# Performance work log

Hardware: AMD Instinct MI355X
Metric: run time of the kernel (lower is better)

The kernel has to match this reference:

```python
import jax, jax.numpy as jnp
import numpy as np

B, T, F, H = 128, 1024, 64, 256


def _lstm_step(h, c, x_t, W_ih, W_hh, b):
    # PyTorch gate order: i, f, g, o ; b = b_ih + b_hh
    g = x_t @ W_ih.T + h @ W_hh.T + b
    i, f, gg, o = jnp.split(g, 4, axis=-1)
    c_new = jax.nn.sigmoid(f) * c + jax.nn.sigmoid(i) * jnp.tanh(gg)
    h_new = jax.nn.sigmoid(o) * jnp.tanh(c_new)
    return h_new, c_new


def setup_inputs() -> dict:
    key = jax.random.key(0)
    ks = jax.random.split(key, 20)
    s = 1.0 / np.sqrt(H)
    u = lambda k, shape: jax.random.uniform(k, shape, jnp.float32, -s, s)
    return {
        "x": jax.random.normal(ks[0], (B, T, F), jnp.float32),
        "eps": jax.random.normal(ks[1], (1, B, H), jnp.float32),
        "enc_W_ih": u(ks[2], (4 * H, F)),
        "enc_W_hh": u(ks[3], (4 * H, H)),
        "enc_b": u(ks[4], (4 * H,)),
        "W_mp": u(ks[5], (H, H)),
        "b_mp": u(ks[6], (H,)),
        "W_lp": u(ks[7], (H, H)),
        "b_lp": u(ks[8], (H,)),
        "dec_W_ih": u(ks[9], (4 * H, H)),
        "dec_W_hh": u(ks[10], (4 * H, H)),
        "dec_b": u(ks[11], (4 * H,)),
        "W_mx": u(ks[12], (F, H)),
        "b_mx": u(ks[13], (F,)),
        "W_lx": u(ks[14], (F, H)),
        "b_lx": u(ks[15], (F,)),
    }


def reference(x, eps, enc_W_ih, enc_W_hh, enc_b, W_mp, b_mp, W_lp, b_lp,
              dec_W_ih, dec_W_hh, dec_b, W_mx, b_mx, W_lx, b_lx):
    Bx = x.shape[0]
    # ---- encoder LSTM over time ----
    def enc_step(carry, x_t):
        h, c = carry
        h, c = _lstm_step(h, c, x_t, enc_W_ih, enc_W_hh, enc_b)
        return (h, c), None
    h0 = jnp.zeros((Bx, H), x.dtype)
    (h_T, _), _ = jax.lax.scan(enc_step, (h0, h0), x.transpose(1, 0, 2))
    h_T = h_T[None]  # [1, B, H] like torch nn.LSTM final h

    # ---- posterior heads + reparameterization ----
    mu_post = h_T @ W_mp.T + b_mp
    logsigma2_post = h_T @ W_lp.T + b_lp
    z0 = eps * jnp.exp(logsigma2_post / 2) + mu_post  # [1, B, H]

    def dec_step(carry, _):
        y, h, c = carry
        h, c = _lstm_step(h, c, y, dec_W_ih, dec_W_hh, dec_b)
        return (h, h, c), h
    y0 = jnp.zeros((Bx, H), x.dtype)
    c0 = jnp.zeros((Bx, H), x.dtype)
    _, ys = jax.lax.scan(dec_step, (y0, z0[0], c0), None, length=T)
    outputs = ys.transpose(1, 0, 2)  # [B, T, H]

    mu_xhat = outputs @ W_mx.T + b_mx            # [B, T, F]
    logsigma2_xhat = outputs @ W_lx.T + b_lx     # [B, T, F]
    return (mu_post, logsigma2_post, mu_xhat, logsigma2_xhat)
```

## Files before the change

kernel.cpp:

```cpp
#include <hip/hip_runtime.h>
#include <stdint.h>

#define Bc 128
#define Tc 1024
#define Fc 64
#define Hc 256

typedef float f32x4 __attribute__((ext_vector_type(4)));
typedef short s16x8 __attribute__((ext_vector_type(8)));

#define MFMA16(a, b, c) __builtin_amdgcn_mfma_f32_16x16x32_bf16((a), (b), (c), 0, 0, 0)

__device__ unsigned long long g_hbuf[2 * Bc * Hc];

__device__ __forceinline__ unsigned short f2bf(float f) {
  unsigned u = __float_as_uint(f);
  u += 0x7FFFu + ((u >> 16) & 1u);
  return (unsigned short)(u >> 16);
}
__device__ __forceinline__ float bf2f(unsigned short h) {
  return __uint_as_float(((unsigned)h) << 16);
}
__device__ __forceinline__ float sigm(float x) { return 1.0f / (1.0f + __expf(-x)); }
__device__ __forceinline__ float tanh2(float x) { return 1.0f - 2.0f / (__expf(2.0f * x) + 1.0f); }

__device__ __forceinline__ void wfrag2(const float* p, s16x8& hi, s16x8& lo) {
#pragma unroll
  for (int j = 0; j < 8; ++j) {
    unsigned short h = f2bf(p[j]);
    hi[j] = (short)h;
    lo[j] = (short)f2bf(p[j] - bf2f(h));
  }
}
__device__ __forceinline__ void wfrag2sum(const float* p, const float* q, s16x8& hi, s16x8& lo) {
#pragma unroll
  for (int j = 0; j < 8; ++j) {
    float v = p[j] + q[j];
    unsigned short h = f2bf(v);
    hi[j] = (short)h;
    lo[j] = (short)f2bf(v - bf2f(h));
  }
}
__device__ __forceinline__ f32x4 splat4(float v) {
  f32x4 r; r[0] = v; r[1] = v; r[2] = v; r[3] = v; return r;
}

extern "C" __global__ void __launch_bounds__(256, 1)
vrae_persistent(const float* __restrict__ x, const float* __restrict__ eps,
                const float* __restrict__ Wih_e, const float* __restrict__ Whh_e,
                const float* __restrict__ b_e,
                const float* __restrict__ Wmp, const float* __restrict__ bmp,
                const float* __restrict__ Wlp, const float* __restrict__ blp,
                const float* __restrict__ Wih_d, const float* __restrict__ Whh_d,
                const float* __restrict__ b_d,
                const float* __restrict__ Wmx, const float* __restrict__ bmx,
                const float* __restrict__ Wlx, const float* __restrict__ blx,
                float* __restrict__ out)
{
  __shared__ unsigned short h_hi[16][264];
  __shared__ unsigned short h_lo[16][264];
  __shared__ unsigned short x_hi[16][72];
  __shared__ unsigned short x_lo[16][72];
  __shared__ float glds[4][16][36];

  unsigned long long* hbuf = g_hbuf;

  const int tid  = threadIdx.x;
  const int wg   = blockIdx.x;
  const int sg   = wg & 7;
  const int gg   = wg >> 3;
  const int wv   = tid >> 6;
  const int l15  = tid & 15;
  const int quad = (tid >> 4) & 3;
  const int s0   = sg * 16;
  const int um   = tid >> 4;
  const int uj   = tid & 15;

  auto consume = [&](int tag) {
    const unsigned long long* src =
        hbuf + (size_t)(tag & 1) * (Bc * Hc) + (size_t)(s0 + um) * Hc;
    unsigned long long w[16];
#pragma unroll
    for (int u = 0; u < 16; ++u)
      w[u] = __hip_atomic_load(src + uj + 16 * u, __ATOMIC_RELAXED, __HIP_MEMORY_SCOPE_AGENT);
    for (;;) {
      bool ok = true;
#pragma unroll
      for (int u = 0; u < 16; ++u) ok = ok && ((w[u] >> 32) == (unsigned long long)(unsigned)tag);
      if (ok) break;
      __builtin_amdgcn_s_sleep(2);
#pragma unroll
      for (int u = 0; u < 16; ++u)
        if ((w[u] >> 32) != (unsigned long long)(unsigned)tag)
          w[u] = __hip_atomic_load(src + uj + 16 * u, __ATOMIC_RELAXED, __HIP_MEMORY_SCOPE_AGENT);
    }
#pragma unroll
    for (int u = 0; u < 16; ++u) {
      h_hi[um][uj + 16 * u] = (unsigned short)(w[u] >> 16);
      h_lo[um][uj + 16 * u] = (unsigned short)(w[u] & 0xFFFFu);
    }
  };

  auto publish_h = [&](int otag, float hv, int jloc) {
    unsigned long long* dst =
        hbuf + (size_t)(otag & 1) * (Bc * Hc) + (size_t)(s0 + um) * Hc + gg * 32 + jloc;
    unsigned short hi = f2bf(hv);
    unsigned short lo = f2bf(hv - bf2f(hi));
    unsigned long long word = ((unsigned long long)(unsigned)otag << 32) |
                              (((unsigned)hi << 16) | (unsigned)lo);
    __hip_atomic_store(dst, word, __ATOMIC_RELAXED, __HIP_MEMORY_SCOPE_AGENT);
  };

  float creg0 = 0.f, creg1 = 0.f;
  auto lstm_update = [&](int otag) {
#pragma unroll
    for (int u = 0; u < 2; ++u) {
      const int j = uj + 16 * u;
      float gi = glds[0][um][j], gf = glds[1][um][j];
      float gc = glds[2][um][j], go = glds[3][um][j];
      float iv = sigm(gi), fv = sigm(gf), cv = tanh2(gc), ov = sigm(go);
      float cr = u ? creg1 : creg0;
      cr = fv * cr + iv * cv;
      float hv = ov * tanh2(cr);
      if (u) creg1 = cr; else creg0 = cr;
      publish_h(otag, hv, j);
    }
  };

  s16x8 wmh[2][8], wml[2][8];
  s16x8 wxh[2][2], wxl[2][2];
  float biasg[2];
#pragma unroll
  for (int ch = 0; ch < 2; ++ch) {
    const int row = wv * 256 + gg * 32 + ch * 16 + l15;
    biasg[ch] = b_e[row];
#pragma unroll
    for (int c = 0; c < 8; ++c)
      wfrag2(Whh_e + (size_t)row * Hc + c * 32 + quad * 8, wmh[ch][c], wml[ch][c]);
#pragma unroll
    for (int c = 0; c < 2; ++c)
      wfrag2(Wih_e + (size_t)row * Fc + c * 32 + quad * 8, wxh[ch][c], wxl[ch][c]);
  }

#pragma unroll
  for (int u = 0; u < 16; ++u) { h_hi[um][uj + 16 * u] = 0; h_lo[um][uj + 16 * u] = 0; }
  __syncthreads();

  for (int it = 0; it < Tc; ++it) {
    {
      const float* xp = x + (size_t)(s0 + um) * (Tc * Fc) + (size_t)it * Fc + uj * 4;
      f32x4 xv = *(const f32x4*)xp;
#pragma unroll
      for (int j = 0; j < 4; ++j) {
        unsigned short h = f2bf(xv[j]);
        x_hi[um][uj * 4 + j] = h;
        x_lo[um][uj * 4 + j] = f2bf(xv[j] - bf2f(h));
      }
    }
    if (it > 0) consume(it);
    __syncthreads();

    f32x4 acc0 = splat4(biasg[0]);
    f32x4 acc1 = splat4(biasg[1]);
#pragma unroll
    for (int c = 0; c < 2; ++c) {
      s16x8 ah = *(const s16x8*)&x_hi[l15][c * 32 + quad * 8];
      s16x8 al = *(const s16x8*)&x_lo[l15][c * 32 + quad * 8];
      acc0 = MFMA16(ah, wxh[0][c], acc0);
      acc0 = MFMA16(ah, wxl[0][c], acc0);
      acc0 = MFMA16(al, wxh[0][c], acc0);
      acc1 = MFMA16(ah, wxh[1][c], acc1);
      acc1 = MFMA16(ah, wxl[1][c], acc1);
      acc1 = MFMA16(al, wxh[1][c], acc1);
    }
#pragma unroll
    for (int c = 0; c < 8; ++c) {
      s16x8 ah = *(const s16x8*)&h_hi[l15][c * 32 + quad * 8];
      s16x8 al = *(const s16x8*)&h_lo[l15][c * 32 + quad * 8];
      acc0 = MFMA16(ah, wmh[0][c], acc0);
      acc0 = MFMA16(ah, wml[0][c], acc0);
      acc0 = MFMA16(al, wmh[0][c], acc0);
      acc1 = MFMA16(ah, wmh[1][c], acc1);
      acc1 = MFMA16(ah, wml[1][c], acc1);
      acc1 = MFMA16(al, wmh[1][c], acc1);
    }
#pragma unroll
    for (int r = 0; r < 4; ++r) {
      glds[wv][quad * 4 + r][l15]      = acc0[r];
      glds[wv][quad * 4 + r][16 + l15] = acc1[r];
    }
    __syncthreads();
    lstm_update(it + 1);
  }

  consume(Tc);
  {
    const float* WM = (wv < 2) ? Wmp : Wlp;
    const float* bM = (wv < 2) ? bmp : blp;
    const int prow = gg * 32 + (wv & 1) * 16 + l15;
    s16x8 wph[8], wpl[8];
#pragma unroll
    for (int c = 0; c < 8; ++c)
      wfrag2(WM + (size_t)prow * Hc + c * 32 + quad * 8, wph[c], wpl[c]);
    const float pb = bM[prow];
    __syncthreads();
    f32x4 acc = splat4(pb);
#pragma unroll
    for (int c = 0; c < 8; ++c) {
      s16x8 ah = *(const s16x8*)&h_hi[l15][c * 32 + quad * 8];
      s16x8 al = *(const s16x8*)&h_lo[l15][c * 32 + quad * 8];
      acc = MFMA16(ah, wph[c], acc);
      acc = MFMA16(ah, wpl[c], acc);
      acc = MFMA16(al, wph[c], acc);
    }
#pragma unroll
    for (int r = 0; r < 4; ++r)
      glds[wv >> 1][quad * 4 + r][(wv & 1) * 16 + l15] = acc[r];
    __syncthreads();
#pragma unroll
    for (int u = 0; u < 2; ++u) {
      const int j  = uj + 16 * u;
      const int jg = gg * 32 + j;
      float mu = glds[0][um][j];
      float lp = glds[1][um][j];
      float ev = eps[(size_t)(s0 + um) * Hc + jg];
      float z  = ev * __expf(0.5f * lp) + mu;
      out[(size_t)(s0 + um) * Hc + jg] = mu;
      out[(size_t)Bc * Hc + (size_t)(s0 + um) * Hc + jg] = lp;
      publish_h(Tc + 1, z, j);
    }
    creg0 = 0.f; creg1 = 0.f;
  }

#pragma unroll
  for (int ch = 0; ch < 2; ++ch) {
    const int row = wv * 256 + gg * 32 + ch * 16 + l15;
    biasg[ch] = b_d[row];
#pragma unroll
    for (int c = 0; c < 8; ++c)
      wfrag2sum(Wih_d + (size_t)row * Hc + c * 32 + quad * 8,
                Whh_d + (size_t)row * Hc + c * 32 + quad * 8,
                wmh[ch][c], wml[ch][c]);
  }
  s16x8 wpjh[8], wpjl[8];
  float pjb;
  {
    const float* WP = (gg < 4) ? Wmx : Wlx;
    const float* bP = (gg < 4) ? bmx : blx;
    const int prow = (gg & 3) * 16 + l15;
    pjb = bP[prow];
#pragma unroll
    for (int c = 0; c < 8; ++c)
      wfrag2(WP + (size_t)prow * Hc + c * 32 + quad * 8, wpjh[c], wpjl[c]);
  }
  const size_t outMu = (size_t)2 * Bc * Hc;
  const size_t outLs = outMu + (size_t)Bc * Tc * Fc;

  for (int it = 0; it <= Tc; ++it) {
    consume(Tc + 1 + it);
    __syncthreads();

    if (it < Tc) {
      f32x4 acc0 = splat4(biasg[0]);
      f32x4 acc1 = splat4(biasg[1]);
      if (it == 0) {
#pragma unroll
        for (int ch = 0; ch < 2; ++ch) {
          const int row = wv * 256 + gg * 32 + ch * 16 + l15;
#pragma unroll
          for (int c = 0; c < 8; ++c) {
            s16x8 wzh, wzl;
            wfrag2(Whh_d + (size_t)row * Hc + c * 32 + quad * 8, wzh, wzl);
            s16x8 ah = *(const s16x8*)&h_hi[l15][c * 32 + quad * 8];
            s16x8 al = *(const s16x8*)&h_lo[l15][c * 32 + quad * 8];
            f32x4& acc = ch ? acc1 : acc0;
            acc = MFMA16(ah, wzh, acc);
            acc = MFMA16(ah, wzl, acc);
            acc = MFMA16(al, wzh, acc);
          }
        }
      } else {
#pragma unroll
        for (int c = 0; c < 8; ++c) {
          s16x8 ah = *(const s16x8*)&h_hi[l15][c * 32 + quad * 8];
          s16x8 al = *(const s16x8*)&h_lo[l15][c * 32 + quad * 8];
          acc0 = MFMA16(ah, wmh[0][c], acc0);
          acc0 = MFMA16(ah, wml[0][c], acc0);
          acc0 = MFMA16(al, wmh[0][c], acc0);
          acc1 = MFMA16(ah, wmh[1][c], acc1);
          acc1 = MFMA16(ah, wml[1][c], acc1);
          acc1 = MFMA16(al, wmh[1][c], acc1);
        }
      }
#pragma unroll
      for (int r = 0; r < 4; ++r) {
        glds[wv][quad * 4 + r][l15]      = acc0[r];
        glds[wv][quad * 4 + r][16 + l15] = acc1[r];
      }
      __syncthreads();
      lstm_update(Tc + 2 + it);
    }

    if (it > 0 && wv == 0) {
      f32x4 acc = splat4(pjb);
#pragma unroll
      for (int c = 0; c < 8; ++c) {
        s16x8 ah = *(const s16x8*)&h_hi[l15][c * 32 + quad * 8];
        s16x8 al = *(const s16x8*)&h_lo[l15][c * 32 + quad * 8];
        acc = MFMA16(ah, wpjh[c], acc);
        acc = MFMA16(ah, wpjl[c], acc);
        acc = MFMA16(al, wpjh[c], acc);
      }
      const size_t base = (gg < 4) ? outMu : outLs;
      const int tout = it - 1;
      const int fcol = (gg & 3) * 16 + l15;
#pragma unroll
      for (int r = 0; r < 4; ++r) {
        const int m = quad * 4 + r;
        out[base + ((size_t)(s0 + m) * Tc + tout) * Fc + fcol] = acc[r];
      }
    }
    __syncthreads();
  }

  {
    const int atag = 2 * Tc + 2;
#pragma unroll
    for (int u = 0; u < 2; ++u) {
      unsigned long long* dst = hbuf + (size_t)(s0 + um) * Hc + gg * 32 + uj + 16 * u;
      __hip_atomic_store(dst, ((unsigned long long)(unsigned)atag << 32),
                         __ATOMIC_RELAXED, __HIP_MEMORY_SCOPE_AGENT);
    }
    consume(atag);
#pragma unroll
    for (int u = 0; u < 2; ++u) {
      unsigned long long* dst =
          hbuf + (size_t)(Bc * Hc) + (size_t)(s0 + um) * Hc + gg * 32 + uj + 16 * u;
      __hip_atomic_store(dst, 0ull, __ATOMIC_RELAXED, __HIP_MEMORY_SCOPE_AGENT);
    }
  }
}

extern "C" void kernel_launch(void* const* d_in, const int* in_sizes, int n_in,
                              void* d_out, int out_size, void* d_ws, size_t ws_size,
                              hipStream_t stream)
{
  (void)in_sizes; (void)n_in; (void)out_size; (void)d_ws; (void)ws_size;

  const float* x     = (const float*)d_in[0];
  const float* eps   = (const float*)d_in[1];
  const float* Wih_e = (const float*)d_in[2];
  const float* Whh_e = (const float*)d_in[3];
  const float* b_e   = (const float*)d_in[4];
  const float* Wmp   = (const float*)d_in[5];
  const float* bmp   = (const float*)d_in[6];
  const float* Wlp   = (const float*)d_in[7];
  const float* blp   = (const float*)d_in[8];
  const float* Wih_d = (const float*)d_in[9];
  const float* Whh_d = (const float*)d_in[10];
  const float* b_d   = (const float*)d_in[11];
  const float* Wmx   = (const float*)d_in[12];
  const float* bmx   = (const float*)d_in[13];
  const float* Wlx   = (const float*)d_in[14];
  const float* blx   = (const float*)d_in[15];
  float* out = (float*)d_out;

  void* args[] = { &x, &eps, &Wih_e, &Whh_e, &b_e, &Wmp, &bmp, &Wlp, &blp,
                   &Wih_d, &Whh_d, &b_d, &Wmx, &bmx, &Wlx, &blx, &out };
  hipError_t err = hipLaunchCooperativeKernel((void*)vrae_persistent, dim3(64), dim3(256),
                                              args, 0, stream);
  if (err != hipSuccess) {
    vrae_persistent<<<dim3(64), dim3(256), 0, stream>>>(
        x, eps, Wih_e, Whh_e, b_e, Wmp, bmp, Wlp, blp,
        Wih_d, Whh_d, b_d, Wmx, bmx, Wlx, blx, out);
  }
}
```

Before: 5.505 ms.

## Interleave gate rows per wave to do LSTM update in registers via shuffles

Weight rows are remapped so each wave's MFMA output holds all four gates for its own 8 hidden columns. The LSTM cell update then runs in registers using lane shuffles instead of staging gates through LDS, which removes one __syncthreads and the LDS round trip per step. h and x LDS buffers are double-buffered by step parity, which lets the trailing barrier in the decoder loop go, and the spin-wait sleep is shortened. The cost is that only half the lanes do the nonlinearity, and parity buffering must stay correct (the projection now reads h_hi[0] after the encoder).

```diff
diff --git a/kernel.cpp b/kernel.cpp
--- a/kernel.cpp
+++ b/kernel.cpp
@@ -57,11 +57,11 @@
                 const float* __restrict__ Wlx, const float* __restrict__ blx,
                 float* __restrict__ out)
 {
-  __shared__ unsigned short h_hi[16][264];
-  __shared__ unsigned short h_lo[16][264];
-  __shared__ unsigned short x_hi[16][72];
-  __shared__ unsigned short x_lo[16][72];
-  __shared__ float glds[4][16][36];
+  __shared__ unsigned short h_hi[2][16][264];
+  __shared__ unsigned short h_lo[2][16][264];
+  __shared__ unsigned short x_hi[2][16][72];
+  __shared__ unsigned short x_lo[2][16][72];
+  __shared__ float glds[2][16][36];
 
   unsigned long long* hbuf = g_hbuf;
 
@@ -75,10 +75,14 @@
   const int s0   = sg * 16;
   const int um   = tid >> 4;
   const int uj   = tid & 15;
+  const int colbase = gg * 32 + wv * 8;
+  const int rowf0 = ((l15 < 8) ? 0 : 256) + colbase + (l15 & 7);
+  const int rowf1 = ((l15 < 8) ? 512 : 768) + colbase + (l15 & 7);
 
   auto consume = [&](int tag) {
+    const int p = tag & 1;
     const unsigned long long* src =
-        hbuf + (size_t)(tag & 1) * (Bc * Hc) + (size_t)(s0 + um) * Hc;
+        hbuf + (size_t)p * (Bc * Hc) + (size_t)(s0 + um) * Hc;
     unsigned long long w[16];
 #pragma unroll
     for (int u = 0; u < 16; ++u)
@@ -88,7 +92,7 @@
 #pragma unroll
       for (int u = 0; u < 16; ++u) ok = ok && ((w[u] >> 32) == (unsigned long long)(unsigned)tag);
       if (ok) break;
-      __builtin_amdgcn_s_sleep(2);
+      __builtin_amdgcn_s_sleep(1);
 #pragma unroll
       for (int u = 0; u < 16; ++u)
         if ((w[u] >> 32) != (unsigned long long)(unsigned)tag)
@@ -96,12 +100,11 @@
     }
 #pragma unroll
     for (int u = 0; u < 16; ++u) {
-      h_hi[um][uj + 16 * u] = (unsigned short)(w[u] >> 16);
-      h_lo[um][uj + 16 * u] = (unsigned short)(w[u] & 0xFFFFu);
+      h_hi[p][um][uj + 16 * u] = (unsigned short)(w[u] >> 16);
+      h_lo[p][um][uj + 16 * u] = (unsigned short)(w[u] & 0xFFFFu);
     }
   };
-
-  auto publish_h = [&](int otag, float hv, int jloc) {
+  auto publish_w = [&](int otag, float hv, int jloc) {
     unsigned long long* dst =
         hbuf + (size_t)(otag & 1) * (Bc * Hc) + (size_t)(s0 + um) * Hc + gg * 32 + jloc;
     unsigned short hi = f2bf(hv);
@@ -111,86 +114,89 @@
     __hip_atomic_store(dst, word, __ATOMIC_RELAXED, __HIP_MEMORY_SCOPE_AGENT);
   };
 
-  float creg0 = 0.f, creg1 = 0.f;
-  auto lstm_update = [&](int otag) {
-#pragma unroll
-    for (int u = 0; u < 2; ++u) {
-      const int j = uj + 16 * u;
-      float gi = glds[0][um][j], gf = glds[1][um][j];
-      float gc = glds[2][um][j], go = glds[3][um][j];
-      float iv = sigm(gi), fv = sigm(gf), cv = tanh2(gc), ov = sigm(go);
-      float cr = u ? creg1 : creg0;
-      cr = fv * cr + iv * cv;
-      float hv = ov * tanh2(cr);
-      if (u) creg1 = cr; else creg0 = cr;
-      publish_h(otag, hv, j);
+  float creg[4] = {0.f, 0.f, 0.f, 0.f};
+  auto update_publish = [&](f32x4 acc0, f32x4 acc1, int otag) {
+    f32x4 r0, r1;
+#pragma unroll
+    for (int r = 0; r < 4; ++r) {
+      r0[r] = __shfl_xor(acc0[r], 8, 64);
+      r1[r] = __shfl_xor(acc1[r], 8, 64);
+    }
+    if (l15 < 8) {
+#pragma unroll
+      for (int r = 0; r < 4; ++r) {
+        float iv = sigm(acc0[r]), fv = sigm(r0[r]);
+        float gv = tanh2(acc1[r]), ov = sigm(r1[r]);
+        float c = fv * creg[r] + iv * gv;
+        creg[r] = c;
+        float hv = ov * tanh2(c);
+        unsigned short hi = f2bf(hv);
+        unsigned short lo = f2bf(hv - bf2f(hi));
+        unsigned long long word = ((unsigned long long)(unsigned)otag << 32) |
+                                  (((unsigned)hi << 16) | (unsigned)lo);
+        __hip_atomic_store(hbuf + (size_t)(otag & 1) * (Bc * Hc) +
+                               (size_t)(s0 + quad * 4 + r) * Hc + colbase + l15,
+                           word, __ATOMIC_RELAXED, __HIP_MEMORY_SCOPE_AGENT);
+      }
     }
   };
 
-  s16x8 wmh[2][8], wml[2][8];
-  s16x8 wxh[2][2], wxl[2][2];
-  float biasg[2];
-#pragma unroll
-  for (int ch = 0; ch < 2; ++ch) {
-    const int row = wv * 256 + gg * 32 + ch * 16 + l15;
-    biasg[ch] = b_e[row];
-#pragma unroll
-    for (int c = 0; c < 8; ++c)
-      wfrag2(Whh_e + (size_t)row * Hc + c * 32 + quad * 8, wmh[ch][c], wml[ch][c]);
-#pragma unroll
-    for (int c = 0; c < 2; ++c)
-      wfrag2(Wih_e + (size_t)row * Fc + c * 32 + quad * 8, wxh[ch][c], wxl[ch][c]);
-  }
-
-#pragma unroll
-  for (int u = 0; u < 16; ++u) { h_hi[um][uj + 16 * u] = 0; h_lo[um][uj + 16 * u] = 0; }
-  __syncthreads();
+  s16x8 bh0[8], bl0[8], bh1[8], bl1[8];
+  s16x8 xbh0[2], xbl0[2], xbh1[2], xbl1[2];
+  float bias0 = b_e[rowf0], bias1 = b_e[rowf1];
+#pragma unroll
+  for (int c = 0; c < 8; ++c) {
+    wfrag2(Whh_e + (size_t)rowf0 * Hc + c * 32 + quad * 8, bh0[c], bl0[c]);
+    wfrag2(Whh_e + (size_t)rowf1 * Hc + c * 32 + quad * 8, bh1[c], bl1[c]);
+  }
+#pragma unroll
+  for (int c = 0; c < 2; ++c) {
+    wfrag2(Wih_e + (size_t)rowf0 * Fc + c * 32 + quad * 8, xbh0[c], xbl0[c]);
+    wfrag2(Wih_e + (size_t)rowf1 * Fc + c * 32 + quad * 8, xbh1[c], xbl1[c]);
+  }
 
   for (int it = 0; it < Tc; ++it) {
+    const int p = it & 1;
     {
       const float* xp = x + (size_t)(s0 + um) * (Tc * Fc) + (size_t)it * Fc + uj * 4;
       f32x4 xv = *(const f32x4*)xp;
 #pragma unroll
       for (int j = 0; j < 4; ++j) {
         unsigned short h = f2bf(xv[j]);
-        x_hi[um][uj * 4 + j] = h;
-        x_lo[um][uj * 4 + j] = f2bf(xv[j] - bf2f(h));
+        x_hi[p][um][uj * 4 + j] = h;
+        x_lo[p][um][uj * 4 + j] = f2bf(xv[j] - bf2f(h));
       }
     }
     if (it > 0) consume(it);
     __syncthreads();
 
-    f32x4 acc0 = splat4(biasg[0]);
-    f32x4 acc1 = splat4(biasg[1]);
+    f32x4 acc0 = splat4(bias0);
+    f32x4 acc1 = splat4(bias1);
 #pragma unroll
     for (int c = 0; c < 2; ++c) {
-      s16x8 ah = *(const s16x8*)&x_hi[l15][c * 32 + quad * 8];
-      s16x8 al = *(const s16x8*)&x_lo[l15][c * 32 + quad * 8];
-      acc0 = MFMA16(ah, wxh[0][c], acc0);
-      acc0 = MFMA16(ah, wxl[0][c], acc0);
-      acc0 = MFMA16(al, wxh[0][c], acc0);
-      acc1 = MFMA16(ah, wxh[1][c], acc1);
-      acc1 = MFMA16(ah, wxl[1][c], acc1);
-      acc1 = MFMA16(al, wxh[1][c], acc1);
-    }
-#pragma unroll
-    for (int c = 0; c < 8; ++c) {
-      s16x8 ah = *(const s16x8*)&h_hi[l15][c * 32 + quad * 8];
-      s16x8 al = *(const s16x8*)&h_lo[l15][c * 32 + quad * 8];
-      acc0 = MFMA16(ah, wmh[0][c], acc0);
-      acc0 = MFMA16(ah, wml[0][c], acc0);
-      acc0 = MFMA16(al, wmh[0][c], acc0);
-      acc1 = MFMA16(ah, wmh[1][c], acc1);
-      acc1 = MFMA16(ah, wml[1][c], acc1);
-      acc1 = MFMA16(al, wmh[1][c], acc1);
-    }
-#pragma unroll
-    for (int r = 0; r < 4; ++r) {
-      glds[wv][quad * 4 + r][l15]      = acc0[r];
-      glds[wv][quad * 4 + r][16 + l15] = acc1[r];
-    }
-    __syncthreads();
-    lstm_update(it + 1);
+      s16x8 ah = *(const s16x8*)&x_hi[p][l15][c * 32 + quad * 8];
+      s16x8 al = *(const s16x8*)&x_lo[p][l15][c * 32 + quad * 8];
+      acc0 = MFMA16(ah, xbh0[c], acc0);
+      acc0 = MFMA16(ah, xbl0[c], acc0);
+      acc0 = MFMA16(al, xbh0[c], acc0);
+      acc1 = MFMA16(ah, xbh1[c], acc1);
+      acc1 = MFMA16(ah, xbl1[c], acc1);
+      acc1 = MFMA16(al, xbh1[c], acc1);
+    }
+    if (it > 0) {
+#pragma unroll
+      for (int c = 0; c < 8; ++c) {
+        s16x8 ah = *(const s16x8*)&h_hi[p][l15][c * 32 + quad * 8];
+        s16x8 al = *(const s16x8*)&h_lo[p][l15][c * 32 + quad * 8];
+        acc0 = MFMA16(ah, bh0[c], acc0);
+        acc0 = MFMA16(ah, bl0[c], acc0);
+        acc0 = MFMA16(al, bh0[c], acc0);
+        acc1 = MFMA16(ah, bh1[c], acc1);
+        acc1 = MFMA16(ah, bl1[c], acc1);
+        acc1 = MFMA16(al, bh1[c], acc1);
+      }
+    }
+    update_publish(acc0, acc1, it + 1);
   }
 
   consume(Tc);
@@ -207,8 +213,8 @@
     f32x4 acc = splat4(pb);
 #pragma unroll
     for (int c = 0; c < 8; ++c) {
-      s16x8 ah = *(const s16x8*)&h_hi[l15][c * 32 + quad * 8];
-      s16x8 al = *(const s16x8*)&h_lo[l15][c * 32 + quad * 8];
+      s16x8 ah = *(const s16x8*)&h_hi[0][l15][c * 32 + quad * 8];
+      s16x8 al = *(const s16x8*)&h_lo[0][l15][c * 32 + quad * 8];
       acc = MFMA16(ah, wph[c], acc);
       acc = MFMA16(ah, wpl[c], acc);
       acc = MFMA16(al, wph[c], acc);
@@ -227,100 +233,90 @@
       float z  = ev * __expf(0.5f * lp) + mu;
       out[(size_t)(s0 + um) * Hc + jg] = mu;
       out[(size_t)Bc * Hc + (size_t)(s0 + um) * Hc + jg] = lp;
-      publish_h(Tc + 1, z, j);
-    }
-    creg0 = 0.f; creg1 = 0.f;
-  }
-
-#pragma unroll
-  for (int ch = 0; ch < 2; ++ch) {
-    const int row = wv * 256 + gg * 32 + ch * 16 + l15;
-    biasg[ch] = b_d[row];
+      publish_w(Tc + 1, z, j);
+    }
+    creg[0] = creg[1] = creg[2] = creg[3] = 0.f;
+  }
+
+  bias0 = b_d[rowf0]; bias1 = b_d[rowf1];
+#pragma unroll
+  for (int c = 0; c < 8; ++c) {
+    wfrag2sum(Wih_d + (size_t)rowf0 * Hc + c * 32 + quad * 8,
+              Whh_d + (size_t)rowf0 * Hc + c * 32 + quad * 8, bh0[c], bl0[c]);
+    wfrag2sum(Wih_d + (size_t)rowf1 * Hc + c * 32 + quad * 8,
+              Whh_d + (size_t)rowf1 * Hc + c * 32 + quad * 8, bh1[c], bl1[c]);
+  }
+  s16x8 pwh[8], pwl[8];
+  float pjb;
+  const int Rrow = gg * 16 + l15;
+  {
+    const float* WP = (Rrow < 64) ? Wmx : Wlx;
+    const int fcol = Rrow & 63;
+    pjb = (Rrow < 64) ? bmx[fcol] : blx[fcol];
 #pragma unroll
     for (int c = 0; c < 8; ++c)
-      wfrag2sum(Wih_d + (size_t)row * Hc + c * 32 + quad * 8,
-                Whh_d + (size_t)row * Hc + c * 32 + quad * 8,
-                wmh[ch][c], wml[ch][c]);
-  }
-  s16x8 wpjh[8], wpjl[8];
-  float pjb;
-  {
-    const float* WP = (gg < 4) ? Wmx : Wlx;
-    const float* bP = (gg < 4) ? bmx : blx;
-    const int prow = (gg & 3) * 16 + l15;
-    pjb = bP[prow];
-#pragma unroll
-    for (int c = 0; c < 8; ++c)
-      wfrag2(WP + (size_t)prow * Hc + c * 32 + quad * 8, wpjh[c], wpjl[c]);
+      wfrag2(WP + (size_t)fcol * Hc + c * 32 + quad * 8, pwh[c], pwl[c]);
   }
   const size_t outMu = (size_t)2 * Bc * Hc;
   const size_t outLs = outMu + (size_t)Bc * Tc * Fc;
+  const size_t pbase = (Rrow < 64) ? outMu : outLs;
+  const int pfcol = Rrow & 63;
 
   for (int it = 0; it <= Tc; ++it) {
-    consume(Tc + 1 + it);
+    const int te = Tc + 1 + it;
+    const int p  = te & 1;
+    consume(te);
     __syncthreads();
 
     if (it < Tc) {
-      f32x4 acc0 = splat4(biasg[0]);
-      f32x4 acc1 = splat4(biasg[1]);
+      f32x4 acc0 = splat4(bias0);
+      f32x4 acc1 = splat4(bias1);
       if (it == 0) {
 #pragma unroll
-        for (int ch = 0; ch < 2; ++ch) {
-          const int row = wv * 256 + gg * 32 + ch * 16 + l15;
-#pragma unroll
-          for (int c = 0; c < 8; ++c) {
-            s16x8 wzh, wzl;
-            wfrag2(Whh_d + (size_t)row * Hc + c * 32 + quad * 8, wzh, wzl);
-            s16x8 ah = *(const s16x8*)&h_hi[l15][c * 32 + quad * 8];
-            s16x8 al = *(const s16x8*)&h_lo[l15][c * 32 + quad * 8];
-            f32x4& acc = ch ? acc1 : acc0;
-            acc = MFMA16(ah, wzh, acc);
-            acc = MFMA16(ah, wzl, acc);
-            acc = MFMA16(al, wzh, acc);
-          }
+        for (int c = 0; c < 8; ++c) {
+          s16x8 zh0, zl0, zh1, zl1;
+          wfrag2(Whh_d + (size_t)rowf0 * Hc + c * 32 + quad * 8, zh0, zl0);
+          wfrag2(Whh_d + (size_t)rowf1 * Hc + c * 32 + quad * 8, zh1, zl1);
+          s16x8 ah = *(const s16x8*)&h_hi[p][l15][c * 32 + quad * 8];
+          s16x8 al = *(const s16x8*)&h_lo[p][l15][c * 32 + quad * 8];
+          acc0 = MFMA16(ah, zh0, acc0);
+          acc0 = MFMA16(ah, zl0, acc0);
+          acc0 = MFMA16(al, zh0, acc0);
+          acc1 = MFMA16(ah, zh1, acc1);
+          acc1 = MFMA16(ah, zl1, acc1);
+          acc1 = MFMA16(al, zh1, acc1);
         }
       } else {
 #pragma unroll
         for (int c = 0; c < 8; ++c) {
-          s16x8 ah = *(const s16x8*)&h_hi[l15][c * 32 + quad * 8];
-          s16x8 al = *(const s16x8*)&h_lo[l15][c * 32 + quad * 8];
-          acc0 = MFMA16(ah, wmh[0][c], acc0);
-          acc0 = MFMA16(ah, wml[0][c], acc0);
-          acc0 = MFMA16(al, wmh[0][c], acc0);
-          acc1 = MFMA16(ah, wmh[1][c], acc1);
-          acc1 = MFMA16(ah, wml[1][c], acc1);
-          acc1 = MFMA16(al, wmh[1][c], acc1);
+          s16x8 ah = *(const s16x8*)&h_hi[p][l15][c * 32 + quad * 8];
+          s16x8 al = *(const s16x8*)&h_lo[p][l15][c * 32 + quad * 8];
+          acc0 = MFMA16(ah, bh0[c], acc0);
+          acc0 = MFMA16(ah, bl0[c], acc0);
+          acc0 = MFMA16(al, bh0[c], acc0);
+          acc1 = MFMA16(ah, bh1[c], acc1);
+          acc1 = MFMA16(ah, bl1[c], acc1);
+          acc1 = MFMA16(al, bh1[c], acc1);
         }
       }
-#pragma unroll
-      for (int r = 0; r < 4; ++r) {
-        glds[wv][quad * 4 + r][l15]      = acc0[r];
-        glds[wv][quad * 4 + r][16 + l15] = acc1[r];
-      }
-      __syncthreads();
-      lstm_update(Tc + 2 + it);
+      update_publish(acc0, acc1, te + 1);
     }
 
     if (it > 0 && wv == 0) {
       f32x4 acc = splat4(pjb);
 #pragma unroll
       for (int c = 0; c < 8; ++c) {
-        s16x8 ah = *(const s16x8*)&h_hi[l15][c * 32 + quad * 8];
-        s16x8 al = *(const s16x8*)&h_lo[l15][c * 32 + quad * 8];
-        acc = MFMA16(ah, wpjh[c], acc);
-        acc = MFMA16(ah, wpjl[c], acc);
-        acc = MFMA16(al, wpjh[c], acc);
-      }
-      const size_t base = (gg < 4) ? outMu : outLs;
+        s16x8 ah = *(const s16x8*)&h_hi[p][l15][c * 32 + quad * 8];
+        s16x8 al = *(const s16x8*)&h_lo[p][l15][c * 32 + quad * 8];
+        acc = MFMA16(ah, pwh[c], acc);
+        acc = MFMA16(ah, pwl[c], acc);
+        acc = MFMA16(al, pwh[c], acc);
+      }
       const int tout = it - 1;
-      const int fcol = (gg & 3) * 16 + l15;
-#pragma unroll
-      for (int r = 0; r < 4; ++r) {
-        const int m = quad * 4 + r;
-        out[base + ((size_t)(s0 + m) * Tc + tout) * Fc + fcol] = acc[r];
-      }
-    }
-    __syncthreads();
+#pragma unroll
+      for (int r = 0; r < 4; ++r)
+        out[pbase + ((size_t)(s0 + quad * 4 + r) * Tc + tout) * Fc + pfcol] = acc[r];
+    }
   }
 
   {
```

New measurement: 6.869 ms. 24.8% more time.
